# Performance work log

Hardware: AMD Instinct MI355X
Metric: run time of the kernel (lower is better)

Reference implementation:

```python
import jax, jax.numpy as jnp
import numpy as np

N = 8192
PT_DIM = 3
ENC_DIM = 384
RADIUS = 0.12
ALPHA = 6.0
SQRT_D = ENC_DIM ** 0.5


def setup_inputs() -> dict:
    key = jax.random.key(0)
    k1, k2 = jax.random.split(key)
    pts = jax.random.uniform(k1, (N, PT_DIM), dtype=jnp.float32)  # points in unit cube
    # A corresponds to the (frozen) random-feature matrix: stacked standard normals * alpha
    A = jax.random.normal(k2, (PT_DIM, ENC_DIM), dtype=jnp.float32) * ALPHA
    return {"pts": pts, "A": A}


def reference(pts, A):
    # Radius-ball adjacency: J[i,j] = 1 if ||pts[i]-pts[j]|| < r (dist^2 < r^2, dist >= 0)
    d2 = jnp.sum((pts[:, None, :] - pts[None, :, :]) ** 2, axis=-1)  # (N, N)
    J = (d2 < RADIUS * RADIUS).astype(pts.dtype)                      # (N, N)

    pA = (pts / RADIUS) @ A            # (N, ENC_DIM)
    c, s = jnp.cos(pA), jnp.sin(pA)    # epA = [cos(pA), sin(pA)]

    # Neighbor aggregation: G = J @ epA, done per real/imag part
    Gr = J @ c                          # (N, ENC_DIM)
    Gi = J @ s

    # Complex phase division: (Gr + i Gi) / (cos + i sin)
    G = jax.lax.complex(Gr, Gi) / jax.lax.complex(c, s)

    # Row-wise normalization to norm sqrt(enc_dim)
    G = G / jnp.linalg.norm(G, axis=-1, keepdims=True) * SQRT_D
    return G
```

## Files before the change

### kernel.cpp

```cpp
#include <hip/hip_runtime.h>
#include <hip/hip_fp16.h>
#include <math.h>

#define N_PTS   8192
#define ENC     384
#define NTHREAD 384
#define NCELL1  8
#define NCELLS  512
#define RADIUS  0.12f
#define MAXU    368
#define NCH_SLAB 384
#define GRID_MAIN (8 * NCH_SLAB)

__device__ __forceinline__ void fast_sincos(float x, float& s, float& c) {
    float rev = x * 0.15915494309189535f;
    rev -= rintf(rev);
    s = __builtin_amdgcn_sinf(rev);
    c = __builtin_amdgcn_cosf(rev);
}

__device__ __forceinline__ int cell_of(float x) {
    int c = (int)(x * 8.0f);
    return min(NCELL1 - 1, max(0, c));
}

static __device__ __forceinline__ unsigned h2u(__half2 h) { union { __half2 h; unsigned u; } x; x.h = h; return x.u; }
static __device__ __forceinline__ __half2 u2h(unsigned u) { union { unsigned u; __half2 h; } x; x.u = u; return x.h; }

static const size_t OFF_CSTART_I = 0;
static const size_t OFF_CURSOR_I = 520;
static const size_t OFF_CELLID_I = 1032;
static const size_t OFF_DESC_I   = 9224;
static const size_t INT_END_B    = 12296u * 4;
static const size_t OFF_SPTS_B   = INT_END_B;
static const size_t OFF_CS_B     = OFF_SPTS_B + 131072;
static const size_t WS_FULL_B    = OFF_CS_B + (size_t)(N_PTS + 1) * ENC * 4;

__global__ __launch_bounds__(512) void k_cellid(const float* __restrict__ pts,
                                                int* __restrict__ cell_id) {
    int i = blockIdx.x * 512 + threadIdx.x;
    if (i >= N_PTS) return;
    cell_id[i] = (cell_of(pts[3 * i + 0]) << 6) | (cell_of(pts[3 * i + 1]) << 3)
               | cell_of(pts[3 * i + 2]);
}

__global__ __launch_bounds__(512) void k_scan(const int* __restrict__ cell_id,
                                              int* __restrict__ cell_start,
                                              int* __restrict__ cursor,
                                              int* __restrict__ desc) {
    __shared__ int cnt_l[512];
    __shared__ int sc[512];
    __shared__ int sch[512];
    const int t = threadIdx.x;
    cnt_l[t] = 0;
    __syncthreads();
    for (int i = t; i < N_PTS; i += 512) atomicAdd(&cnt_l[cell_id[i]], 1);
    __syncthreads();
    const int c = cnt_l[t];

    sc[t] = c;
    __syncthreads();
    for (int off = 1; off < 512; off <<= 1) {
        int v = (t >= off) ? sc[t - off] : 0;
        __syncthreads();
        sc[t] += v;
        __syncthreads();
    }
    cell_start[t] = sc[t] - c;
    cursor[t]     = sc[t] - c;
    if (t == 511) cell_start[NCELLS] = sc[511];

    const int nch = (c + 3) >> 2;
    sch[t] = nch;
    __syncthreads();
    for (int off = 1; off < 64; off <<= 1) {
        int v = ((t & 63) >= off) ? sch[t - off] : 0;
        __syncthreads();
        sch[t] += v;
        __syncthreads();
    }
    const int rank = sch[t] - nch;

    for (int i = t; i < GRID_MAIN; i += 512) desc[i] = -1;
    __syncthreads();
    const int slab = t >> 6;
    for (int k = 0; k < nch; ++k) {
        int pos = rank + k;
        if (pos < NCH_SLAB) desc[slab + 8 * pos] = (t << 6) | k;
    }
}

__global__ __launch_bounds__(512) void k_scatter(const float* __restrict__ pts,
                                                 const int* __restrict__ cell_id,
                                                 int* __restrict__ cursor,
                                                 float4* __restrict__ spts) {
    int i = blockIdx.x * 512 + threadIdx.x;
    if (i >= N_PTS) return;
    int pos = atomicAdd(&cursor[cell_id[i]], 1);
    spts[pos] = make_float4(pts[3 * i + 0], pts[3 * i + 1], pts[3 * i + 2],
                            __int_as_float(i));
}

__global__ __launch_bounds__(NTHREAD) void k_encode(const float4* __restrict__ spts,
                                                    const float* __restrict__ A,
                                                    __half2* __restrict__ cs) {
    const int t  = threadIdx.x;
    const int p0 = blockIdx.x * 8;
    const float a0 = A[t], a1 = A[ENC + t], a2 = A[2 * ENC + t];
    #pragma unroll
    for (int k = 0; k < 8; ++k) {
        int p = p0 + k;
        if (p > N_PTS) break;
        if (p == N_PTS) {
            cs[(size_t)p * ENC + t] = __floats2half2_rn(0.f, 0.f);
            break;
        }
        float4 P = spts[p];
        float qx = __fdiv_rn(P.x, RADIUS);
        float qy = __fdiv_rn(P.y, RADIUS);
        float qz = __fdiv_rn(P.z, RADIUS);
        float pa = fmaf(qz, a2, fmaf(qy, a1, qx * a0));
        float s, c;
        fast_sincos(pa, s, c);
        cs[(size_t)p * ENC + t] = __floats2half2_rn(c, s);
    }
}

__global__ __launch_bounds__(NTHREAD) void k_main(const float4* __restrict__ spts,
                                                  const int* __restrict__ cell_start,
                                                  const int* __restrict__ desc_g,
                                                  const uint4* __restrict__ cs4,
                                                  float* __restrict__ out, int out_mode) {
    const int d = desc_g[blockIdx.x];
    if (d < 0) return;
    const int cell = d >> 6;
    const int kk   = d & 63;
    const int t = threadIdx.x, lane = t & 63, wv = t >> 6;
    const int g = t / 96, q = t - g * 96;

    __shared__ int    run_lo[9], run_hi[9];
    __shared__ float4 own_l[4];
    __shared__ int    ne;
    __shared__ __align__(16) unsigned int ent_g[4][96];
    __shared__ uint4  comb_a[4][96];
    __shared__ uint4  comb_b[4][96];
    __shared__ float  red2[4][96];
    __shared__ float  scale_l[4];

    const int o_lo = cell_start[cell];
    const int o_hi = cell_start[cell + 1];
    const int pbase = o_lo + (kk << 2);
    const int np = min(4, o_hi - pbase);

    const int cx = cell >> 6, cy = (cell >> 3) & 7, cz = cell & 7;
    if (t < 9) {
        int dx = t / 3 - 1, dy = t % 3 - 1;
        int cxx = cx + dx, cyy = cy + dy;
        int lo = 0, hi = 0;
        if (cxx >= 0 && cxx <= 7 && cyy >= 0 && cyy <= 7) {
            int basec = (cxx * 8 + cyy) * 8;
            int zlo = max(cz - 1, 0), zhi = min(cz + 1, 7);
            lo = cell_start[basec + zlo];
            hi = cell_start[basec + zhi + 1];
        }
        run_lo[t] = lo; run_hi[t] = hi;
    }
    if (t == 0) ne = 0;
    if (t < 4) {
        int idx = pbase + t;
        own_l[t] = (idx < o_hi) ? spts[idx] : make_float4(1e9f, 1e9f, 1e9f, 0.f);
    }
    __syncthreads();
    const float4 O0 = own_l[0], O1 = own_l[1], O2 = own_l[2], O3 = own_l[3];

    const double R2 = (double)0.12 * (double)0.12;
    const float R2_LO = 0.0144f - 1e-6f;
    const float R2_HI = 0.0144f + 1e-6f;
    const uint4* csq = cs4 + q;

    for (int r = wv; r < 9; r += 6) {
        const int lo = run_lo[r], hi = run_hi[r];
        for (int jb = lo; jb < hi; jb += 64) {
            int j = jb + lane;
            unsigned mk = 0;
            if (j < hi) {
                float4 Pj = spts[j];
                #define TEST(O, BIT) { \
                    float fdx = Pj.x - O.x, fdy = Pj.y - O.y, fdz = Pj.z - O.z; \
                    float d2f = fmaf(fdx, fdx, fmaf(fdy, fdy, fdz * fdz)); \
                    if (d2f < R2_LO) mk |= (BIT); \
                    else if (d2f <= R2_HI) { \
                        double ddx = (double)Pj.x - (double)O.x; \
                        double ddy = (double)Pj.y - (double)O.y; \
                        double ddz = (double)Pj.z - (double)O.z; \
                        if (ddx * ddx + ddy * ddy + ddz * ddz < R2) mk |= (BIT); \
                    } }
                TEST(O0, 1u) TEST(O1, 2u) TEST(O2, 4u) TEST(O3, 8u)
                #undef TEST
            }
            unsigned long long mask = __ballot(mk != 0);
            if (mask) {
                int leader = __ffsll((long long)mask) - 1;
                int basep = 0;
                if (lane == leader) basep = atomicAdd(&ne, __popcll(mask));
                basep = __shfl(basep, leader);
                if (mk != 0) {
                    int pos = basep + __popcll(mask & ((1ull << lane) - 1ull));
                    if (pos < MAXU) ent_g[pos & 3][pos >> 2] = (unsigned)j | (mk << 16);
                }
            }
        }
    }
    __syncthreads();
    const int ne_p  = min(ne, MAXU);
    const int total = (ne_p + 15) & ~15;
    if (t < total - ne_p) {
        int pos = ne_p + t;
        ent_g[pos & 3][pos >> 2] = (unsigned)N_PTS;
    }
    __syncthreads();
    const int P = total >> 2;

    __half2 ax0[4], ax1[4], ax2[4], ax3[4];
    #pragma unroll
    for (int dd = 0; dd < 4; ++dd) {
        ax0[dd] = u2h(0u); ax1[dd] = u2h(0u); ax2[dd] = u2h(0u); ax3[dd] = u2h(0u);
    }
    for (int m = 0; m < P; m += 4) {
        uint4 ev = *(const uint4*)&ent_g[g][m];
        uint4 r0 = csq[(size_t)(ev.x & 0xFFFFu) * 96];
        uint4 r1 = csq[(size_t)(ev.y & 0xFFFFu) * 96];
        uint4 r2 = csq[(size_t)(ev.z & 0xFFFFu) * 96];
        uint4 r3 = csq[(size_t)(ev.w & 0xFFFFu) * 96];
        #define ACC4(R, MK) { \
            unsigned mk_ = (MK); \
            __half2 h0 = u2h((mk_ & 1u) ? 0x3C003C00u : 0u); \
            __half2 h1 = u2h((mk_ & 2u) ? 0x3C003C00u : 0u); \
            __half2 h2 = u2h((mk_ & 4u) ? 0x3C003C00u : 0u); \
            __half2 h3 = u2h((mk_ & 8u) ? 0x3C003C00u : 0u); \
            __half2 rx = u2h(R.x), ry = u2h(R.y), rz = u2h(R.z), rw = u2h(R.w); \
            ax0[0] = __hfma2(rx, h0, ax0[0]); ax0[1] = __hfma2(ry, h0, ax0[1]); \
            ax0[2] = __hfma2(rz, h0, ax0[2]); ax0[3] = __hfma2(rw, h0, ax0[3]); \
            ax1[0] = __hfma2(rx, h1, ax1[0]); ax1[1] = __hfma2(ry, h1, ax1[1]); \
            ax1[2] = __hfma2(rz, h1, ax1[2]); ax1[3] = __hfma2(rw, h1, ax1[3]); \
            ax2[0] = __hfma2(rx, h2, ax2[0]); ax2[1] = __hfma2(ry, h2, ax2[1]); \
            ax2[2] = __hfma2(rz, h2, ax2[2]); ax2[3] = __hfma2(rw, h2, ax2[3]); \
            ax3[0] = __hfma2(rx, h3, ax3[0]); ax3[1] = __hfma2(ry, h3, ax3[1]); \
            ax3[2] = __hfma2(rz, h3, ax3[2]); ax3[3] = __hfma2(rw, h3, ax3[3]); }
        ACC4(r0, ev.x >> 16) ACC4(r1, ev.y >> 16) ACC4(r2, ev.z >> 16) ACC4(r3, ev.w >> 16)
        #undef ACC4
    }

    #define PACK4(A) make_uint4(h2u(A[0]), h2u(A[1]), h2u(A[2]), h2u(A[3]))
    #define ADDU(A, V) { A[0] = __hadd2(A[0], u2h(V.x)); A[1] = __hadd2(A[1], u2h(V.y)); \
                         A[2] = __hadd2(A[2], u2h(V.z)); A[3] = __hadd2(A[3], u2h(V.w)); }
    if (g == 1) { comb_a[0][q] = PACK4(ax0); comb_a[1][q] = PACK4(ax1);
                  comb_a[2][q] = PACK4(ax2); comb_a[3][q] = PACK4(ax3); }
    else if (g == 3) { comb_b[0][q] = PACK4(ax0); comb_b[1][q] = PACK4(ax1);
                       comb_b[2][q] = PACK4(ax2); comb_b[3][q] = PACK4(ax3); }
    __syncthreads();
    if (g == 0) { uint4 v0 = comb_a[0][q], v1 = comb_a[1][q], v2 = comb_a[2][q], v3 = comb_a[3][q];
                  ADDU(ax0, v0) ADDU(ax1, v1) ADDU(ax2, v2) ADDU(ax3, v3) }
    else if (g == 2) { uint4 v0 = comb_b[0][q], v1 = comb_b[1][q], v2 = comb_b[2][q], v3 = comb_b[3][q];
                       ADDU(ax0, v0) ADDU(ax1, v1) ADDU(ax2, v2) ADDU(ax3, v3) }
    __syncthreads();
    if (g == 2) { comb_a[0][q] = PACK4(ax0); comb_a[1][q] = PACK4(ax1);
                  comb_a[2][q] = PACK4(ax2); comb_a[3][q] = PACK4(ax3); }
    __syncthreads();
    if (g == 0) {
        uint4 v0 = comb_a[0][q], v1 = comb_a[1][q], v2 = comb_a[2][q], v3 = comb_a[3][q];
        ADDU(ax0, v0) ADDU(ax1, v1) ADDU(ax2, v2) ADDU(ax3, v3)
        #define NORM_P(AC, PP) { float m2 = 0.f; \
            _Pragma("unroll") for (int dd = 0; dd < 4; ++dd) { \
                float2 f = __half22float2(AC[dd]); \
                m2 = fmaf(f.x, f.x, fmaf(f.y, f.y, m2)); } \
            red2[PP][q] = m2; }
        NORM_P(ax0, 0) NORM_P(ax1, 1) NORM_P(ax2, 2) NORM_P(ax3, 3)
        #undef NORM_P
    }
    #undef PACK4
    #undef ADDU
    __syncthreads();
    if (t < 256) {
        int w = t >> 6, l = t & 63;
        float v = red2[w][l] + (l < 32 ? red2[w][64 + l] : 0.f);
        #pragma unroll
        for (int off = 32; off > 0; off >>= 1) v += __shfl_down(v, off);
        if (l == 0) scale_l[w] = sqrtf(384.0f / v);
    }
    __syncthreads();
    if (g == 0) {
        #define STORE_P(AC, PP) if ((PP) < np) { \
            const float scl = scale_l[PP]; \
            uint4 ov = csq[(size_t)(pbase + (PP)) * 96]; \
            float2 o0 = __half22float2(u2h(ov.x)), o1 = __half22float2(u2h(ov.y)); \
            float2 o2 = __half22float2(u2h(ov.z)), o3 = __half22float2(u2h(ov.w)); \
            float2 g0v = __half22float2(AC[0]), g1v = __half22float2(AC[1]); \
            float2 g2v = __half22float2(AC[2]), g3v = __half22float2(AC[3]); \
            float re0 = (g0v.x * o0.x + g0v.y * o0.y) * scl, im0 = (g0v.y * o0.x - g0v.x * o0.y) * scl; \
            float re1 = (g1v.x * o1.x + g1v.y * o1.y) * scl, im1 = (g1v.y * o1.x - g1v.x * o1.y) * scl; \
            float re2 = (g2v.x * o2.x + g2v.y * o2.y) * scl, im2 = (g2v.y * o2.x - g2v.x * o2.y) * scl; \
            float re3 = (g3v.x * o3.x + g3v.y * o3.y) * scl, im3 = (g3v.y * o3.x - g3v.x * o3.y) * scl; \
            const int o = __float_as_int(own_l[PP].w); \
            if (out_mode == 0) { \
                ((float4*)out)[(size_t)o * 96 + q] = make_float4(re0, re1, re2, re3); \
            } else { \
                ((float4*)out)[(size_t)o * 192 + 2 * q + 0] = make_float4(re0, im0, re1, im1); \
                ((float4*)out)[(size_t)o * 192 + 2 * q + 1] = make_float4(re2, im2, re3, im3); \
            } }
        STORE_P(ax0, 0) STORE_P(ax1, 1) STORE_P(ax2, 2) STORE_P(ax3, 3)
        #undef STORE_P
    }
}

__global__ __launch_bounds__(NTHREAD) void vecKM_allpairs(const float* __restrict__ pts,
                                                          const float* __restrict__ A,
                                                          float* __restrict__ out, int out_mode) {
    const int i = blockIdx.x;
    const int t = threadIdx.x;
    __shared__ float nb_x[512], nb_y[512], nb_z[512];
    __shared__ int nb_cnt;
    __shared__ float red[8];
    if (t == 0) nb_cnt = 0;
    __syncthreads();
    const float xi = pts[3 * i + 0], yi = pts[3 * i + 1], zi = pts[3 * i + 2];
    const double dxi = xi, dyi = yi, dzi = zi;
    const double R2 = (double)0.12 * (double)0.12;
    const float R2_LO = 0.0144f - 1e-6f, R2_HI = 0.0144f + 1e-6f;
    const int lane = t & 63;
    for (int jb = 0; jb < N_PTS; jb += NTHREAD) {
        const int j = jb + t;
        bool isnb = false;
        float xj = 0.f, yj = 0.f, zj = 0.f;
        if (j < N_PTS) {
            xj = pts[3 * j + 0]; yj = pts[3 * j + 1]; zj = pts[3 * j + 2];
            float fdx = xj - xi, fdy = yj - yi, fdz = zj - zi;
            float d2f = fmaf(fdx, fdx, fmaf(fdy, fdy, fdz * fdz));
            if (d2f < R2_LO) isnb = true;
            else if (d2f <= R2_HI) {
                double dx = (double)xj - dxi, dy = (double)yj - dyi, dz = (double)zj - dzi;
                isnb = (dx * dx + dy * dy + dz * dz) < R2;
            }
        }
        unsigned long long mask = __ballot(isnb);
        if (mask) {
            int leader = __ffsll((long long)mask) - 1;
            int basep = 0;
            if (lane == leader) basep = atomicAdd(&nb_cnt, __popcll(mask));
            basep = __shfl(basep, leader);
            if (isnb) {
                int pos = basep + __popcll(mask & ((1ull << lane) - 1ull));
                if (pos < 512) {
                    nb_x[pos] = (xj - xi) * (1.0f / 0.12f);
                    nb_y[pos] = (yj - yi) * (1.0f / 0.12f);
                    nb_z[pos] = (zj - zi) * (1.0f / 0.12f);
                }
            }
        }
    }
    __syncthreads();
    const int nn = min(nb_cnt, 512);
    const float a0 = A[t], a1 = A[ENC + t], a2 = A[2 * ENC + t];
    float gr = 0.f, gi = 0.f;
    #pragma unroll 4
    for (int m = 0; m < nn; ++m) {
        float pa = fmaf(nb_z[m], a2, fmaf(nb_y[m], a1, nb_x[m] * a0));
        float sv, cv;
        fast_sincos(pa, sv, cv);
        gr += cv; gi += sv;
    }
    float m2 = fmaf(gr, gr, gi * gi);
    #pragma unroll
    for (int off = 32; off > 0; off >>= 1) m2 += __shfl_down(m2, off);
    const int wid = t >> 6;
    if (lane == 0) red[wid] = m2;
    __syncthreads();
    if (t == 0) {
        float tot = 0.f;
        for (int w = 0; w < NTHREAD / 64; ++w) tot += red[w];
        red[7] = tot;
    }
    __syncthreads();
    const float scale = sqrtf(384.0f / red[7]);
    const float re = gr * scale, im = gi * scale;
    if (out_mode == 0) out[i * ENC + t] = re;
    else ((float2*)out)[i * ENC + t] = make_float2(re, im);
}

extern "C" void kernel_launch(void* const* d_in, const int* in_sizes, int n_in,
                              void* d_out, int out_size, void* d_ws, size_t ws_size,
                              hipStream_t stream) {
    const float* pts = (const float*)d_in[0];
    const float* A   = (const float*)d_in[1];
    float* out = (float*)d_out;
    const int out_mode = (out_size >= 2 * N_PTS * ENC) ? 1 : 0;

    if (ws_size >= WS_FULL_B) {
        int*     cell_start = (int*)d_ws + OFF_CSTART_I;
        int*     cursor     = (int*)d_ws + OFF_CURSOR_I;
        int*     cell_id    = (int*)d_ws + OFF_CELLID_I;
        int*     desc       = (int*)d_ws + OFF_DESC_I;
        float4*  spts       = (float4*)((char*)d_ws + OFF_SPTS_B);
        __half2* cs         = (__half2*)((char*)d_ws + OFF_CS_B);

        k_cellid<<<16, 512, 0, stream>>>(pts, cell_id);
        k_scan<<<1, 512, 0, stream>>>(cell_id, cell_start, cursor, desc);
        k_scatter<<<16, 512, 0, stream>>>(pts, cell_id, cursor, spts);
        k_encode<<<(N_PTS / 8) + 1, NTHREAD, 0, stream>>>(spts, A, cs);
        k_main<<<GRID_MAIN, NTHREAD, 0, stream>>>(spts, cell_start, desc,
                                                  (const uint4*)cs, out, out_mode);
    } else {
        vecKM_allpairs<<<N_PTS, NTHREAD, 0, stream>>>(pts, A, out, out_mode);
    }
}
```

Before: 72.14 us.

## Tile eight query points per block and fold cell-id into scan kernel

```diff
diff --git a/kernel.cpp b/kernel.cpp
--- a/kernel.cpp
+++ b/kernel.cpp
@@ -8,8 +8,10 @@
 #define NCELL1  8
 #define NCELLS  512
 #define RADIUS  0.12f
-#define MAXU    368
-#define NCH_SLAB 384
+#define TILE8   8
+#define MAXU    496
+#define ENTCAP  124
+#define NCH_SLAB 256
 #define GRID_MAIN (8 * NCH_SLAB)
 
 __device__ __forceinline__ void fast_sincos(float x, float& s, float& c) {
@@ -31,20 +33,13 @@
 static const size_t OFF_CURSOR_I = 520;
 static const size_t OFF_CELLID_I = 1032;
 static const size_t OFF_DESC_I   = 9224;
-static const size_t INT_END_B    = 12296u * 4;
+static const size_t INT_END_B    = 11272u * 4;
 static const size_t OFF_SPTS_B   = INT_END_B;
 static const size_t OFF_CS_B     = OFF_SPTS_B + 131072;
 static const size_t WS_FULL_B    = OFF_CS_B + (size_t)(N_PTS + 1) * ENC * 4;
 
-__global__ __launch_bounds__(512) void k_cellid(const float* __restrict__ pts,
-                                                int* __restrict__ cell_id) {
-    int i = blockIdx.x * 512 + threadIdx.x;
-    if (i >= N_PTS) return;
-    cell_id[i] = (cell_of(pts[3 * i + 0]) << 6) | (cell_of(pts[3 * i + 1]) << 3)
-               | cell_of(pts[3 * i + 2]);
-}
-
-__global__ __launch_bounds__(512) void k_scan(const int* __restrict__ cell_id,
+__global__ __launch_bounds__(512) void k_scan(const float* __restrict__ pts,
+                                              int* __restrict__ cell_id,
                                               int* __restrict__ cell_start,
                                               int* __restrict__ cursor,
                                               int* __restrict__ desc) {
@@ -54,7 +49,14 @@
     const int t = threadIdx.x;
     cnt_l[t] = 0;
     __syncthreads();
-    for (int i = t; i < N_PTS; i += 512) atomicAdd(&cnt_l[cell_id[i]], 1);
+    #pragma unroll
+    for (int k = 0; k < 16; ++k) {
+        int i = t + k * 512;
+        int cid = (cell_of(pts[3 * i + 0]) << 6) | (cell_of(pts[3 * i + 1]) << 3)
+                | cell_of(pts[3 * i + 2]);
+        cell_id[i] = cid;
+        atomicAdd(&cnt_l[cid], 1);
+    }
     __syncthreads();
     const int c = cnt_l[t];
 
@@ -70,7 +72,7 @@
     cursor[t]     = sc[t] - c;
     if (t == 511) cell_start[NCELLS] = sc[511];
 
-    const int nch = (c + 3) >> 2;
+    const int nch = (c + 7) >> 3;
     sch[t] = nch;
     __syncthreads();
     for (int off = 1; off < 64; off <<= 1) {
@@ -139,18 +141,18 @@
     const int g = t / 96, q = t - g * 96;
 
     __shared__ int    run_lo[9], run_hi[9];
-    __shared__ float4 own_l[4];
+    __shared__ float4 own_l[TILE8];
     __shared__ int    ne;
-    __shared__ __align__(16) unsigned int ent_g[4][96];
-    __shared__ uint4  comb_a[4][96];
-    __shared__ uint4  comb_b[4][96];
-    __shared__ float  red2[4][96];
-    __shared__ float  scale_l[4];
+    __shared__ __align__(16) unsigned int ent_g[4][ENTCAP];
+    __shared__ uint4  comb_a[TILE8][96];
+    __shared__ uint4  comb_b[TILE8][96];
+    __shared__ float  red2[TILE8][96];
+    __shared__ float  scale_l[TILE8];
 
     const int o_lo = cell_start[cell];
     const int o_hi = cell_start[cell + 1];
-    const int pbase = o_lo + (kk << 2);
-    const int np = min(4, o_hi - pbase);
+    const int pbase = o_lo + (kk << 3);
+    const int np = min(TILE8, o_hi - pbase);
 
     const int cx = cell >> 6, cy = (cell >> 3) & 7, cz = cell & 7;
     if (t < 9) {
@@ -166,12 +168,13 @@
         run_lo[t] = lo; run_hi[t] = hi;
     }
     if (t == 0) ne = 0;
-    if (t < 4) {
+    if (t < TILE8) {
         int idx = pbase + t;
         own_l[t] = (idx < o_hi) ? spts[idx] : make_float4(1e9f, 1e9f, 1e9f, 0.f);
     }
     __syncthreads();
     const float4 O0 = own_l[0], O1 = own_l[1], O2 = own_l[2], O3 = own_l[3];
+    const float4 O4 = own_l[4], O5 = own_l[5], O6 = own_l[6], O7 = own_l[7];
 
     const double R2 = (double)0.12 * (double)0.12;
     const float R2_LO = 0.0144f - 1e-6f;
@@ -195,7 +198,8 @@
                         double ddz = (double)Pj.z - (double)O.z; \
                         if (ddx * ddx + ddy * ddy + ddz * ddz < R2) mk |= (BIT); \
                     } }
-                TEST(O0, 1u) TEST(O1, 2u) TEST(O2, 4u) TEST(O3, 8u)
+                TEST(O0, 1u)  TEST(O1, 2u)  TEST(O2, 4u)  TEST(O3, 8u)
+                TEST(O4, 16u) TEST(O5, 32u) TEST(O6, 64u) TEST(O7, 128u)
                 #undef TEST
             }
             unsigned long long mask = __ballot(mk != 0);
@@ -213,7 +217,7 @@
     }
     __syncthreads();
     const int ne_p  = min(ne, MAXU);
-    const int total = (ne_p + 15) & ~15;
+    const int total = min((ne_p + 15) & ~15, MAXU);
     if (t < total - ne_p) {
         int pos = ne_p + t;
         ent_g[pos & 3][pos >> 2] = (unsigned)N_PTS;
@@ -221,95 +225,118 @@
     __syncthreads();
     const int P = total >> 2;
 
-    __half2 ax0[4], ax1[4], ax2[4], ax3[4];
+    __half2 ax[TILE8][4];
     #pragma unroll
-    for (int dd = 0; dd < 4; ++dd) {
-        ax0[dd] = u2h(0u); ax1[dd] = u2h(0u); ax2[dd] = u2h(0u); ax3[dd] = u2h(0u);
-    }
+    for (int pp = 0; pp < TILE8; ++pp)
+        #pragma unroll
+        for (int dd = 0; dd < 4; ++dd) ax[pp][dd] = u2h(0u);
+
     for (int m = 0; m < P; m += 4) {
         uint4 ev = *(const uint4*)&ent_g[g][m];
         uint4 r0 = csq[(size_t)(ev.x & 0xFFFFu) * 96];
         uint4 r1 = csq[(size_t)(ev.y & 0xFFFFu) * 96];
         uint4 r2 = csq[(size_t)(ev.z & 0xFFFFu) * 96];
         uint4 r3 = csq[(size_t)(ev.w & 0xFFFFu) * 96];
-        #define ACC4(R, MK) { \
+        #define ACCP(PP) { \
+            __half2 hh = u2h(((mk_ >> PP) & 1u) ? 0x3C003C00u : 0u); \
+            ax[PP][0] = __hfma2(rx, hh, ax[PP][0]); ax[PP][1] = __hfma2(ry, hh, ax[PP][1]); \
+            ax[PP][2] = __hfma2(rz, hh, ax[PP][2]); ax[PP][3] = __hfma2(rw, hh, ax[PP][3]); }
+        #define ACCROW(R, MK) { \
             unsigned mk_ = (MK); \
-            __half2 h0 = u2h((mk_ & 1u) ? 0x3C003C00u : 0u); \
-            __half2 h1 = u2h((mk_ & 2u) ? 0x3C003C00u : 0u); \
-            __half2 h2 = u2h((mk_ & 4u) ? 0x3C003C00u : 0u); \
-            __half2 h3 = u2h((mk_ & 8u) ? 0x3C003C00u : 0u); \
             __half2 rx = u2h(R.x), ry = u2h(R.y), rz = u2h(R.z), rw = u2h(R.w); \
-            ax0[0] = __hfma2(rx, h0, ax0[0]); ax0[1] = __hfma2(ry, h0, ax0[1]); \
-            ax0[2] = __hfma2(rz, h0, ax0[2]); ax0[3] = __hfma2(rw, h0, ax0[3]); \
-            ax1[0] = __hfma2(rx, h1, ax1[0]); ax1[1] = __hfma2(ry, h1, ax1[1]); \
-            ax1[2] = __hfma2(rz, h1, ax1[2]); ax1[3] = __hfma2(rw, h1, ax1[3]); \
-            ax2[0] = __hfma2(rx, h2, ax2[0]); ax2[1] = __hfma2(ry, h2, ax2[1]); \
-            ax2[2] = __hfma2(rz, h2, ax2[2]); ax2[3] = __hfma2(rw, h2, ax2[3]); \
-            ax3[0] = __hfma2(rx, h3, ax3[0]); ax3[1] = __hfma2(ry, h3, ax3[1]); \
-            ax3[2] = __hfma2(rz, h3, ax3[2]); ax3[3] = __hfma2(rw, h3, ax3[3]); }
-        ACC4(r0, ev.x >> 16) ACC4(r1, ev.y >> 16) ACC4(r2, ev.z >> 16) ACC4(r3, ev.w >> 16)
-        #undef ACC4
-    }
-
-    #define PACK4(A) make_uint4(h2u(A[0]), h2u(A[1]), h2u(A[2]), h2u(A[3]))
-    #define ADDU(A, V) { A[0] = __hadd2(A[0], u2h(V.x)); A[1] = __hadd2(A[1], u2h(V.y)); \
-                         A[2] = __hadd2(A[2], u2h(V.z)); A[3] = __hadd2(A[3], u2h(V.w)); }
-    if (g == 1) { comb_a[0][q] = PACK4(ax0); comb_a[1][q] = PACK4(ax1);
-                  comb_a[2][q] = PACK4(ax2); comb_a[3][q] = PACK4(ax3); }
-    else if (g == 3) { comb_b[0][q] = PACK4(ax0); comb_b[1][q] = PACK4(ax1);
-                       comb_b[2][q] = PACK4(ax2); comb_b[3][q] = PACK4(ax3); }
-    __syncthreads();
-    if (g == 0) { uint4 v0 = comb_a[0][q], v1 = comb_a[1][q], v2 = comb_a[2][q], v3 = comb_a[3][q];
-                  ADDU(ax0, v0) ADDU(ax1, v1) ADDU(ax2, v2) ADDU(ax3, v3) }
-    else if (g == 2) { uint4 v0 = comb_b[0][q], v1 = comb_b[1][q], v2 = comb_b[2][q], v3 = comb_b[3][q];
-                       ADDU(ax0, v0) ADDU(ax1, v1) ADDU(ax2, v2) ADDU(ax3, v3) }
-    __syncthreads();
-    if (g == 2) { comb_a[0][q] = PACK4(ax0); comb_a[1][q] = PACK4(ax1);
-                  comb_a[2][q] = PACK4(ax2); comb_a[3][q] = PACK4(ax3); }
+            ACCP(0) ACCP(1) ACCP(2) ACCP(3) ACCP(4) ACCP(5) ACCP(6) ACCP(7) }
+        ACCROW(r0, ev.x >> 16) ACCROW(r1, ev.y >> 16)
+        ACCROW(r2, ev.z >> 16) ACCROW(r3, ev.w >> 16)
+        #undef ACCROW
+        #undef ACCP
+    }
+
+    if (g == 1) {
+        #pragma unroll
+        for (int pp = 0; pp < TILE8; ++pp)
+            comb_a[pp][q] = make_uint4(h2u(ax[pp][0]), h2u(ax[pp][1]), h2u(ax[pp][2]), h2u(ax[pp][3]));
+    } else if (g == 3) {
+        #pragma unroll
+        for (int pp = 0; pp < TILE8; ++pp)
+            comb_b[pp][q] = make_uint4(h2u(ax[pp][0]), h2u(ax[pp][1]), h2u(ax[pp][2]), h2u(ax[pp][3]));
+    }
     __syncthreads();
     if (g == 0) {
-        uint4 v0 = comb_a[0][q], v1 = comb_a[1][q], v2 = comb_a[2][q], v3 = comb_a[3][q];
-        ADDU(ax0, v0) ADDU(ax1, v1) ADDU(ax2, v2) ADDU(ax3, v3)
-        #define NORM_P(AC, PP) { float m2 = 0.f; \
-            _Pragma("unroll") for (int dd = 0; dd < 4; ++dd) { \
-                float2 f = __half22float2(AC[dd]); \
-                m2 = fmaf(f.x, f.x, fmaf(f.y, f.y, m2)); } \
-            red2[PP][q] = m2; }
-        NORM_P(ax0, 0) NORM_P(ax1, 1) NORM_P(ax2, 2) NORM_P(ax3, 3)
-        #undef NORM_P
-    }
-    #undef PACK4
-    #undef ADDU
+        #pragma unroll
+        for (int pp = 0; pp < TILE8; ++pp) {
+            uint4 v = comb_a[pp][q];
+            ax[pp][0] = __hadd2(ax[pp][0], u2h(v.x)); ax[pp][1] = __hadd2(ax[pp][1], u2h(v.y));
+            ax[pp][2] = __hadd2(ax[pp][2], u2h(v.z)); ax[pp][3] = __hadd2(ax[pp][3], u2h(v.w));
+        }
+    } else if (g == 2) {
+        #pragma unroll
+        for (int pp = 0; pp < TILE8; ++pp) {
+            uint4 v = comb_b[pp][q];
+            ax[pp][0] = __hadd2(ax[pp][0], u2h(v.x)); ax[pp][1] = __hadd2(ax[pp][1], u2h(v.y));
+            ax[pp][2] = __hadd2(ax[pp][2], u2h(v.z)); ax[pp][3] = __hadd2(ax[pp][3], u2h(v.w));
+        }
+    }
+    __syncthreads();
+    if (g == 2) {
+        #pragma unroll
+        for (int pp = 0; pp < TILE8; ++pp)
+            comb_a[pp][q] = make_uint4(h2u(ax[pp][0]), h2u(ax[pp][1]), h2u(ax[pp][2]), h2u(ax[pp][3]));
+    }
+    __syncthreads();
+    if (g == 0) {
+        #pragma unroll
+        for (int pp = 0; pp < TILE8; ++pp) {
+            uint4 v = comb_a[pp][q];
+            ax[pp][0] = __hadd2(ax[pp][0], u2h(v.x)); ax[pp][1] = __hadd2(ax[pp][1], u2h(v.y));
+            ax[pp][2] = __hadd2(ax[pp][2], u2h(v.z)); ax[pp][3] = __hadd2(ax[pp][3], u2h(v.w));
+        }
+        #pragma unroll
+        for (int pp = 0; pp < TILE8; ++pp) {
+            float m2 = 0.f;
+            #pragma unroll
+            for (int dd = 0; dd < 4; ++dd) {
+                float2 f = __half22float2(ax[pp][dd]);
+                m2 = fmaf(f.x, f.x, fmaf(f.y, f.y, m2));
+            }
+            red2[pp][q] = m2;
+        }
+    }
     __syncthreads();
     if (t < 256) {
         int w = t >> 6, l = t & 63;
-        float v = red2[w][l] + (l < 32 ? red2[w][64 + l] : 0.f);
-        #pragma unroll
-        for (int off = 32; off > 0; off >>= 1) v += __shfl_down(v, off);
-        if (l == 0) scale_l[w] = sqrtf(384.0f / v);
+        #pragma unroll
+        for (int h = 0; h < 2; ++h) {
+            int pp = w + 4 * h;
+            float v = red2[pp][l] + (l < 32 ? red2[pp][64 + l] : 0.f);
+            #pragma unroll
+            for (int off = 32; off > 0; off >>= 1) v += __shfl_down(v, off);
+            if (l == 0) scale_l[pp] = sqrtf(384.0f / v);
+        }
     }
     __syncthreads();
     if (g == 0) {
-        #define STORE_P(AC, PP) if ((PP) < np) { \
-            const float scl = scale_l[PP]; \
-            uint4 ov = csq[(size_t)(pbase + (PP)) * 96]; \
-            float2 o0 = __half22float2(u2h(ov.x)), o1 = __half22float2(u2h(ov.y)); \
-            float2 o2 = __half22float2(u2h(ov.z)), o3 = __half22float2(u2h(ov.w)); \
-            float2 g0v = __half22float2(AC[0]), g1v = __half22float2(AC[1]); \
-            float2 g2v = __half22float2(AC[2]), g3v = __half22float2(AC[3]); \
-            float re0 = (g0v.x * o0.x + g0v.y * o0.y) * scl, im0 = (g0v.y * o0.x - g0v.x * o0.y) * scl; \
-            float re1 = (g1v.x * o1.x + g1v.y * o1.y) * scl, im1 = (g1v.y * o1.x - g1v.x * o1.y) * scl; \
-            float re2 = (g2v.x * o2.x + g2v.y * o2.y) * scl, im2 = (g2v.y * o2.x - g2v.x * o2.y) * scl; \
-            float re3 = (g3v.x * o3.x + g3v.y * o3.y) * scl, im3 = (g3v.y * o3.x - g3v.x * o3.y) * scl; \
-            const int o = __float_as_int(own_l[PP].w); \
-            if (out_mode == 0) { \
-                ((float4*)out)[(size_t)o * 96 + q] = make_float4(re0, re1, re2, re3); \
-            } else { \
-                ((float4*)out)[(size_t)o * 192 + 2 * q + 0] = make_float4(re0, im0, re1, im1); \
-                ((float4*)out)[(size_t)o * 192 + 2 * q + 1] = make_float4(re2, im2, re3, im3); \
-            } }
-        STORE_P(ax0, 0) STORE_P(ax1, 1) STORE_P(ax2, 2) STORE_P(ax3, 3)
-        #undef STORE_P
+        #pragma unroll
+        for (int pp = 0; pp < TILE8; ++pp) {
+            if (pp < np) {
+                const float scl = scale_l[pp];
+                uint4 ov = csq[(size_t)(pbase + pp) * 96];
+                float2 o0 = __half22float2(u2h(ov.x)), o1 = __half22float2(u2h(ov.y));
+                float2 o2 = __half22float2(u2h(ov.z)), o3 = __half22float2(u2h(ov.w));
+                float2 g0v = __half22float2(ax[pp][0]), g1v = __half22float2(ax[pp][1]);
+                float2 g2v = __half22float2(ax[pp][2]), g3v = __half22float2(ax[pp][3]);
+                float re0 = (g0v.x * o0.x + g0v.y * o0.y) * scl, im0 = (g0v.y * o0.x - g0v.x * o0.y) * scl;
+                float re1 = (g1v.x * o1.x + g1v.y * o1.y) * scl, im1 = (g1v.y * o1.x - g1v.x * o1.y) * scl;
+                float re2 = (g2v.x * o2.x + g2v.y * o2.y) * scl, im2 = (g2v.y * o2.x - g2v.x * o2.y) * scl;
+                float re3 = (g3v.x * o3.x + g3v.y * o3.y) * scl, im3 = (g3v.y * o3.x - g3v.x * o3.y) * scl;
+                const int o = __float_as_int(own_l[pp].w);
+                if (out_mode == 0) {
+                    ((float4*)out)[(size_t)o * 96 + q] = make_float4(re0, re1, re2, re3);
+                } else {
+                    ((float4*)out)[(size_t)o * 192 + 2 * q + 0] = make_float4(re0, im0, re1, im1);
+                    ((float4*)out)[(size_t)o * 192 + 2 * q + 1] = make_float4(re2, im2, re3, im3);
+                }
+            }
+        }
     }
 }
 
@@ -403,8 +430,7 @@
         float4*  spts       = (float4*)((char*)d_ws + OFF_SPTS_B);
         __half2* cs         = (__half2*)((char*)d_ws + OFF_CS_B);
 
-        k_cellid<<<16, 512, 0, stream>>>(pts, cell_id);
-        k_scan<<<1, 512, 0, stream>>>(cell_id, cell_start, cursor, desc);
+        k_scan<<<1, 512, 0, stream>>>(pts, cell_id, cell_start, cursor, desc);
         k_scatter<<<16, 512, 0, stream>>>(pts, cell_id, cursor, spts);
         k_encode<<<(N_PTS / 8) + 1, NTHREAD, 0, stream>>>(spts, A, cs);
         k_main<<<GRID_MAIN, NTHREAD, 0, stream>>>(spts, cell_start, desc,
```

Result: slower. 82.74 us (+14.7%).

## Fuse cell-id, scan and scatter into a single preprocessing kernel

Applied to the files above, without the earlier changes.

```diff
diff --git a/kernel.cpp b/kernel.cpp
--- a/kernel.cpp
+++ b/kernel.cpp
@@ -28,33 +28,35 @@
 static __device__ __forceinline__ __half2 u2h(unsigned u) { union { unsigned u; __half2 h; } x; x.u = u; return x.h; }
 
 static const size_t OFF_CSTART_I = 0;
-static const size_t OFF_CURSOR_I = 520;
-static const size_t OFF_CELLID_I = 1032;
-static const size_t OFF_DESC_I   = 9224;
-static const size_t INT_END_B    = 12296u * 4;
-static const size_t OFF_SPTS_B   = INT_END_B;
+static const size_t OFF_DESC_I   = 520;
+static const size_t INT_END_B    = 3600u * 4;
+static const size_t OFF_SPTS_B   = 14400;
 static const size_t OFF_CS_B     = OFF_SPTS_B + 131072;
 static const size_t WS_FULL_B    = OFF_CS_B + (size_t)(N_PTS + 1) * ENC * 4;
 
-__global__ __launch_bounds__(512) void k_cellid(const float* __restrict__ pts,
-                                                int* __restrict__ cell_id) {
-    int i = blockIdx.x * 512 + threadIdx.x;
-    if (i >= N_PTS) return;
-    cell_id[i] = (cell_of(pts[3 * i + 0]) << 6) | (cell_of(pts[3 * i + 1]) << 3)
-               | cell_of(pts[3 * i + 2]);
-}
-
-__global__ __launch_bounds__(512) void k_scan(const int* __restrict__ cell_id,
+__global__ __launch_bounds__(512) void k_prep(const float* __restrict__ pts,
                                               int* __restrict__ cell_start,
-                                              int* __restrict__ cursor,
-                                              int* __restrict__ desc) {
+                                              int* __restrict__ desc,
+                                              float4* __restrict__ spts) {
     __shared__ int cnt_l[512];
     __shared__ int sc[512];
     __shared__ int sch[512];
+    __shared__ int cur_l[512];
     const int t = threadIdx.x;
     cnt_l[t] = 0;
     __syncthreads();
-    for (int i = t; i < N_PTS; i += 512) atomicAdd(&cnt_l[cell_id[i]], 1);
+
+    float xs[16], ys[16], zs[16];
+    int   cids[16];
+    #pragma unroll
+    for (int k = 0; k < 16; ++k) {
+        int i = t + k * 512;
+        float x = pts[3 * i + 0], y = pts[3 * i + 1], z = pts[3 * i + 2];
+        xs[k] = x; ys[k] = y; zs[k] = z;
+        int cid = (cell_of(x) << 6) | (cell_of(y) << 3) | cell_of(z);
+        cids[k] = cid;
+        atomicAdd(&cnt_l[cid], 1);
+    }
     __syncthreads();
     const int c = cnt_l[t];
 
@@ -67,7 +69,7 @@
         __syncthreads();
     }
     cell_start[t] = sc[t] - c;
-    cursor[t]     = sc[t] - c;
+    cur_l[t]      = sc[t] - c;
     if (t == 511) cell_start[NCELLS] = sc[511];
 
     const int nch = (c + 3) >> 2;
@@ -88,17 +90,13 @@
         int pos = rank + k;
         if (pos < NCH_SLAB) desc[slab + 8 * pos] = (t << 6) | k;
     }
-}
-
-__global__ __launch_bounds__(512) void k_scatter(const float* __restrict__ pts,
-                                                 const int* __restrict__ cell_id,
-                                                 int* __restrict__ cursor,
-                                                 float4* __restrict__ spts) {
-    int i = blockIdx.x * 512 + threadIdx.x;
-    if (i >= N_PTS) return;
-    int pos = atomicAdd(&cursor[cell_id[i]], 1);
-    spts[pos] = make_float4(pts[3 * i + 0], pts[3 * i + 1], pts[3 * i + 2],
-                            __int_as_float(i));
+
+    #pragma unroll
+    for (int k = 0; k < 16; ++k) {
+        int i = t + k * 512;
+        int pos = atomicAdd(&cur_l[cids[k]], 1);
+        spts[pos] = make_float4(xs[k], ys[k], zs[k], __int_as_float(i));
+    }
 }
 
 __global__ __launch_bounds__(NTHREAD) void k_encode(const float4* __restrict__ spts,
@@ -397,15 +395,11 @@
 
     if (ws_size >= WS_FULL_B) {
         int*     cell_start = (int*)d_ws + OFF_CSTART_I;
-        int*     cursor     = (int*)d_ws + OFF_CURSOR_I;
-        int*     cell_id    = (int*)d_ws + OFF_CELLID_I;
         int*     desc       = (int*)d_ws + OFF_DESC_I;
         float4*  spts       = (float4*)((char*)d_ws + OFF_SPTS_B);
         __half2* cs         = (__half2*)((char*)d_ws + OFF_CS_B);
 
-        k_cellid<<<16, 512, 0, stream>>>(pts, cell_id);
-        k_scan<<<1, 512, 0, stream>>>(cell_id, cell_start, cursor, desc);
-        k_scatter<<<16, 512, 0, stream>>>(pts, cell_id, cursor, spts);
+        k_prep<<<1, 512, 0, stream>>>(pts, cell_start, desc, spts);
         k_encode<<<(N_PTS / 8) + 1, NTHREAD, 0, stream>>>(spts, A, cs);
         k_main<<<GRID_MAIN, NTHREAD, 0, stream>>>(spts, cell_start, desc,
                                                   (const uint4*)cs, out, out_mode);
```

New measurement: 67.54 us. -6.4%, faster.
